# Kernel optimization log

Hardware: AMD Instinct MI355X
Metric: run time of the kernel (lower is better)

## Reference

```python
import jax, jax.numpy as jnp
import numpy as np

B, S, E, H = 4, 2048, 1024, 16
D = E // H  # head dim = 64


def setup_inputs() -> dict:
    key = jax.random.key(0)
    ks = jax.random.split(key, 9)
    sc = 1.0 / np.sqrt(E)
    x = jax.random.normal(ks[0], (B, S, E), dtype=jnp.float32)
    # causal mask: 1 = keep, 0 = masked -> -inf (matches masked_fill(mask==0, -inf))
    mask = jnp.broadcast_to(jnp.tril(jnp.ones((S, S), dtype=jnp.int32)), (B, S, S))
    return {
        "x": x,
        "mask": mask,
        "wq": jax.random.normal(ks[1], (E, E), dtype=jnp.float32) * sc,
        "bq": jax.random.normal(ks[2], (E,), dtype=jnp.float32) * sc,
        "wk": jax.random.normal(ks[3], (E, E), dtype=jnp.float32) * sc,
        "bk": jax.random.normal(ks[4], (E,), dtype=jnp.float32) * sc,
        "wv": jax.random.normal(ks[5], (E, E), dtype=jnp.float32) * sc,
        "bv": jax.random.normal(ks[6], (E,), dtype=jnp.float32) * sc,
        "wo": jax.random.normal(ks[7], (E, E), dtype=jnp.float32) * sc,
        "bo": jax.random.normal(ks[8], (E,), dtype=jnp.float32) * sc,
    }


def reference(x, mask, wq, bq, wk, bk, wv, bv, wo, bo):
    # nn.Linear: y = x @ W^T + b
    def proj(w, b):
        y = jnp.einsum('bse,fe->bsf', x, w) + b
        return y.reshape(B, S, H, D).transpose(0, 2, 1, 3)  # [B,H,S,D]

    q = proj(wq, bq)
    k = proj(wk, bk)
    v = proj(wv, bv)
    denom = jnp.asarray(np.sqrt(D), dtype=x.dtype)
    score = jnp.einsum('bhqd,bhkd->bhqk', q, k) / denom  # [B,H,S,S]
    score = jnp.where(mask[:, None, :, :] == 0, jnp.asarray(-jnp.inf, score.dtype), score)
    attn = jax.nn.softmax(score, axis=-1)
    out = jnp.einsum('bhqk,bhkd->bhqd', attn, v)  # [B,H,S,D]
    out = out.transpose(0, 2, 1, 3).reshape(B, S, E)
    return jnp.einsum('bse,fe->bsf', out, wo) + bo
```

## Files before the change

kernel.cpp:

```cpp
#include <hip/hip_runtime.h>
#include <cstdint>
#include <cstddef>

typedef unsigned short u16;
typedef __bf16 bf16;
typedef bf16 bf16x8 __attribute__((ext_vector_type(8)));
typedef bf16 bf16x4 __attribute__((ext_vector_type(4)));
typedef float f32x4 __attribute__((ext_vector_type(4)));
typedef u16 u16x8 __attribute__((ext_vector_type(8)));
typedef u16 u16x4 __attribute__((ext_vector_type(4)));

#define ASYNC16(g, l) __builtin_amdgcn_global_load_lds( \
    (const __attribute__((address_space(1))) void*)(g), \
    (__attribute__((address_space(3))) void*)(l), 16, 0, 0)

#define FENCE asm volatile("" ::: "memory")
#define BARRIER do { FENCE; __builtin_amdgcn_s_barrier(); FENCE; } while (0)
#define WAITVM(n) asm volatile("s_waitcnt vmcnt(" #n ")" ::: "memory")

__device__ __forceinline__ u16 f2bf(float f) {
  bf16 h = (bf16)f;
  return __builtin_bit_cast(u16, h);
}

__device__ __forceinline__ u16x4 pk4(float a, float b, float c, float d) {
  bf16x4 v = { (bf16)a, (bf16)b, (bf16)c, (bf16)d };
  return __builtin_bit_cast(u16x4, v);
}

__device__ __forceinline__ void store_out(u16* p, float v) { *p = f2bf(v); }
__device__ __forceinline__ void store_out(float* p, float v) { *p = v; }

__device__ __forceinline__ f32x4 mfma16(bf16x8 a, bf16x8 b, f32x4 c) {
  return __builtin_amdgcn_mfma_f32_16x16x32_bf16(a, b, c, 0, 0, 0);
}

__global__ void prep(const float* __restrict__ x,  const float* __restrict__ wq,
                     const float* __restrict__ wk, const float* __restrict__ wv,
                     const float* __restrict__ wo, const float* __restrict__ bq,
                     const float* __restrict__ bk,
                     u16* __restrict__ xb, u16* __restrict__ wqkb,
                     u16* __restrict__ wvb, u16* __restrict__ wob,
                     float* __restrict__ bqk, float scl)
{
  const int bid = blockIdx.x, tid = threadIdx.x;
  if (bid < 8192) {
    int i = bid * 256 + tid;
    float4 v = ((const float4*)x)[i];
    ((u16x4*)xb)[i] = pk4(v.x, v.y, v.z, v.w);
  } else if (bid < 12288) {
    int wsel = (bid - 8192) >> 10;
    int i = ((bid - 8192) & 1023) * 256 + tid;
    const float* src = wsel == 0 ? wq : wsel == 1 ? wk : wsel == 2 ? wv : wo;
    u16* dst = wsel == 0 ? wqkb : wsel == 1 ? wqkb + 1048576 : wsel == 2 ? wvb : wob;
    float s = wsel == 0 ? scl : 1.0f;
    float4 v = ((const float4*)src)[i];
    ((u16x4*)dst)[i] = pk4(v.x * s, v.y * s, v.z * s, v.w * s);
  } else {
    for (int i = tid; i < 1024; i += 256) {
      bqk[i] = bq[i] * scl;
      bqk[1024 + i] = bk[i];
    }
  }
}

template <typename OutT>
__device__ __forceinline__ void gemm128(
    u16* sA, u16* sB,
    const u16* __restrict__ A, const u16* __restrict__ Bm,
    const float* __restrict__ bias_col, const float* __restrict__ bias_row,
    OutT* __restrict__ C, int M, int N, int K, int bm, int bn)
{
  const int tid = threadIdx.x;
  const int w = tid >> 6, lane = tid & 63;
  const int quad = lane >> 4, l15 = lane & 15;
  const int wr = w >> 2, wc = w & 3;

  const int srow = tid >> 3;
  const int sslot = (tid & 7) ^ (srow & 7);
  const u16* gA = A + (size_t)(bm * 128 + srow) * K + sslot * 8;
  const u16* gB = Bm + (size_t)(bn * 256 + srow) * K + sslot * 8;
  u16* dA = sA + tid * 8;
  u16* dB = sB + tid * 8;
  const size_t rK64 = (size_t)64 * K;

  auto stage0 = [&](int c, int kt) {
    const u16* a = gA + kt * 64;
    u16* da = dA + c * 8192;
    ASYNC16(a, da);
    ASYNC16(a + rK64, da + 4096);
    ASYNC16(gB + kt * 64, dB + c * 16384);
  };
  auto stage1 = [&](int c, int kt) {
    const u16* b = gB + kt * 64;
    u16* db = dB + c * 16384;
    ASYNC16(b + rK64,     db + 4096);
    ASYNC16(b + 2 * rK64, db + 8192);
    ASYNC16(b + 3 * rK64, db + 12288);
  };

  f32x4 acc[4][4] = {};
  bf16x8 af[4][2];
  bf16x8 bfr[2][2];

  const int aRow = (wr * 64 + l15) * 64;
  const int bRow = (wc * 64 + l15) * 64;
  const int sw0 = (quad ^ (l15 & 7)) * 8;

#define LDA(SRC) do { \
    _Pragma("unroll") \
    for (int i = 0; i < 4; i++) { \
      af[i][0] = *(const bf16x8*)((SRC) + aRow + i * 1024 + sw0); \
      af[i][1] = *(const bf16x8*)((SRC) + aRow + i * 1024 + (sw0 ^ 32)); \
    } } while (0)

#define LDB(SRC, NH) do { \
    _Pragma("unroll") \
    for (int j = 0; j < 2; j++) { \
      bfr[j][0] = *(const bf16x8*)((SRC) + bRow + ((NH)*2 + j) * 1024 + sw0); \
      bfr[j][1] = *(const bf16x8*)((SRC) + bRow + ((NH)*2 + j) * 1024 + (sw0 ^ 32)); \
    } } while (0)

#define MMQ(NH) do { \
    __builtin_amdgcn_s_setprio(1); \
    _Pragma("unroll") \
    for (int i = 0; i < 4; i++) { \
      acc[i][(NH)*2+0] = mfma16(af[i][0], bfr[0][0], acc[i][(NH)*2+0]); \
      acc[i][(NH)*2+0] = mfma16(af[i][1], bfr[0][1], acc[i][(NH)*2+0]); \
      acc[i][(NH)*2+1] = mfma16(af[i][0], bfr[1][0], acc[i][(NH)*2+1]); \
      acc[i][(NH)*2+1] = mfma16(af[i][1], bfr[1][1], acc[i][(NH)*2+1]); \
    } \
    __builtin_amdgcn_s_setprio(0); \
  } while (0)

  const int NT = K >> 6;

  stage0(0, 0); stage1(0, 0);
  stage0(1, 1); stage1(1, 1);
  WAITVM(6);
  BARRIER;

  for (int t = 0; t < NT; ++t) {
    const int c = t % 3, c2 = (t + 2) % 3;
    const bool more = (t + 2 < NT);
    const u16* SA = sA + c * 8192;
    const u16* SB = sB + c * 16384;

    LDA(SA); LDB(SB, 0);
    if (more) stage0(c2, t + 2);
    BARRIER;
    MMQ(0);
    BARRIER;

    LDB(SB, 1);
    if (more) {
      stage1(c2, t + 2);
      WAITVM(6);
    } else if (t == NT - 2) {
      WAITVM(0);
    }
    BARRIER;
    MMQ(1);
    BARRIER;
  }

#pragma unroll
  for (int nh = 0; nh < 2; nh++) {
#pragma unroll
    for (int j = 0; j < 2; j++) {
      const int cc = bn * 256 + wc * 64 + nh * 32 + j * 16 + l15;
      const float bc = bias_col ? bias_col[cc] : 0.f;
#pragma unroll
      for (int i = 0; i < 4; i++) {
        const int r0 = bm * 128 + wr * 64 + i * 16 + quad * 4;
        f32x4 v = acc[i][nh * 2 + j];
#pragma unroll
        for (int ri = 0; ri < 4; ri++) {
          const float bb = bc + (bias_row ? bias_row[r0 + ri] : 0.f);
          store_out(&C[(size_t)(r0 + ri) * N + cc], v[ri] + bb);
        }
      }
    }
  }
#undef LDA
#undef LDB
#undef MMQ
}

__global__ __launch_bounds__(512, 2) void gemm_qkv(
    const u16* __restrict__ xb, const u16* __restrict__ wqkb,
    const u16* __restrict__ wvb, const float* __restrict__ bqk,
    const float* __restrict__ bv, u16* __restrict__ qk, u16* __restrict__ vt)
{
  __shared__ __align__(16) u16 sA[3 * 8192];
  __shared__ __align__(16) u16 sB[3 * 16384];
  const int id = blockIdx.x;
  if (id < 512) {
    gemm128<u16>(sA, sB, xb, wqkb, bqk, nullptr, qk, 8192, 2048, 1024,
                 id >> 3, id & 7);
  } else {
    const int j = id - 512;
    gemm128<u16>(sA, sB, wvb, xb, nullptr, bv, vt, 1024, 8192, 1024,
                 j & 7, j >> 3);
  }
}

__global__ __launch_bounds__(512, 2) void gemm_out(
    const u16* __restrict__ ctx, const u16* __restrict__ wob,
    const float* __restrict__ bo, float* __restrict__ out)
{
  __shared__ __align__(16) u16 sA[3 * 8192];
  __shared__ __align__(16) u16 sB[3 * 16384];
  const int id = blockIdx.x;
  gemm128<float>(sA, sB, ctx, wob, bo, nullptr, out, 8192, 1024, 1024,
                 id >> 2, id & 3);
}

__global__ __launch_bounds__(512, 2) void fattn(
    const u16* __restrict__ QK, const u16* __restrict__ VT, u16* __restrict__ ctx)
{
  __shared__ u16 Kt[2][128 * 64];
  __shared__ u16 Vt[2][64 * 128];
  __shared__ u16 Pt[8 * 32 * 32];

  const int tid = threadIdx.x;
  const int w = tid >> 6, lane = tid & 63;
  const int quad = lane >> 4, l15 = lane & 15;
  const int bx = blockIdx.x, h = blockIdx.y, b = blockIdx.z;
  const int P8[8] = {7, 0, 6, 1, 5, 2, 4, 3};
  const int tq = (b & 2) ? 7 - P8[bx] : P8[bx];
  const int qbase = tq * 256 + w * 32;

  const int kr = tid >> 3, kc = (tid & 7) ^ (kr & 7);
  const int vr = tid >> 4, vc = (tid & 15) ^ (vr & 15);

  const u16* QKb = QK + (size_t)b * 2048 * 2048;
  const u16* Kg = QKb + 1024 + h * 64 + kc * 8;
  const u16* Vg = VT + (size_t)(h * 64) * 8192 + b * 2048 + vc * 8;

  u16* Pw = Pt + w * 1024;

  bf16x8 ones;
#pragma unroll
  for (int j = 0; j < 8; j++) ones[j] = (bf16)1.0f;

  bf16x8 qf[2][2];
#pragma unroll
  for (int mt = 0; mt < 2; mt++)
#pragma unroll
    for (int ks = 0; ks < 2; ks++)
      qf[mt][ks] = *(const bf16x8*)(QKb + (size_t)(qbase + mt * 16 + l15) * 2048 +
                                    h * 64 + ks * 32 + quad * 8);

  auto stage = [&](int bi, int t) {
#pragma unroll
    for (int s = 0; s < 2; s++) {
      ASYNC16(Kg + (size_t)(t * 128 + s * 64 + kr) * 2048, Kt[bi] + (s * 512 + w * 64) * 8);
      ASYNC16(Vg + (size_t)(s * 32 + vr) * 8192 + t * 128,  Vt[bi] + (s * 512 + w * 64) * 8);
    }
  };

  f32x4 oacc[4][2] = {};
  f32x4 lacc[2] = {};

  const int tmax = 2 * tq + 1;
  stage(0, 0);

  for (int t = 0; t <= tmax; t++) {
    const int cur = t & 1;
    if (t < tmax) { stage(cur ^ 1, t + 1); WAITVM(4); }
    else          { WAITVM(0); }
    BARRIER;

    const u16* Kc = Kt[cur];
    const u16* Vc = Vt[cur];

    f32x4 st[2][8] = {};
#pragma unroll
    for (int ks = 0; ks < 2; ks++) {
      bf16x8 kf[8];
#pragma unroll
      for (int nt = 0; nt < 8; nt++) {
        int row = nt * 16 + l15;
        kf[nt] = *(const bf16x8*)(Kc + (row * 8 + ((ks * 4 + quad) ^ (row & 7))) * 8);
      }
#pragma unroll
      for (int nt = 0; nt < 8; nt++) {
        st[0][nt] = mfma16(kf[nt], qf[0][ks], st[0][nt]);
        st[1][nt] = mfma16(kf[nt], qf[1][ks], st[1][nt]);
      }
    }

    if (t >= 2 * tq) {
#pragma unroll
      for (int mt = 0; mt < 2; mt++) {
        const int qg = qbase + mt * 16 + l15;
#pragma unroll
        for (int nt = 0; nt < 8; nt++)
#pragma unroll
          for (int r = 0; r < 4; r++)
            if (t * 128 + nt * 16 + quad * 4 + r > qg) st[mt][nt][r] = -3e38f;
      }
    }
#pragma unroll
    for (int mt = 0; mt < 2; mt++)
#pragma unroll
      for (int nt = 0; nt < 8; nt++)
#pragma unroll
        for (int r = 0; r < 4; r++)
          st[mt][nt][r] = exp2f(st[mt][nt][r]);

#pragma unroll
    for (int hf = 0; hf < 2; hf++) {
#pragma unroll
      for (int ks = 0; ks < 2; ks++) {
#pragma unroll
        for (int mt = 0; mt < 2; mt++) {
          const int row = mt * 16 + l15;
          const int swz = (row >> 1) & 3;
#pragma unroll
          for (int j = 0; j < 2; j++) {
            int nt = hf * 4 + ks * 2 + j;
            u16x4 pkv = pk4(st[mt][nt][0], st[mt][nt][1], st[mt][nt][2], st[mt][nt][3]);
            int c = (j * 2 + (quad >> 1)) ^ swz;
            *(u16x4*)(Pw + (row << 5) + (c << 3) + ((quad & 1) << 2)) = pkv;
          }
        }
        const int cq = quad ^ ((l15 >> 1) & 3);
        bf16x8 pf0 = *(const bf16x8*)(Pw + (l15 << 5) + (cq << 3));
        bf16x8 pf1 = *(const bf16x8*)(Pw + ((16 + l15) << 5) + (cq << 3));
        lacc[0] = mfma16(ones, pf0, lacc[0]);
        lacc[1] = mfma16(ones, pf1, lacc[1]);
#pragma unroll
        for (int dt = 0; dt < 4; dt++) {
          int row = dt * 16 + l15;
          bf16x8 vf = *(const bf16x8*)(Vc + (row * 16 + ((hf * 8 + ks * 4 + quad) ^ (row & 15))) * 8);
          oacc[dt][0] = mfma16(vf, pf0, oacc[dt][0]);
          oacc[dt][1] = mfma16(vf, pf1, oacc[dt][1]);
        }
      }
    }
    BARRIER;
  }

#pragma unroll
  for (int mt = 0; mt < 2; mt++) {
    float rl = 1.0f / lacc[mt][0];
    size_t row = (size_t)b * 2048 + qbase + mt * 16 + l15;
#pragma unroll
    for (int dt = 0; dt < 4; dt++) {
      u16x4 o = pk4(oacc[dt][mt][0] * rl, oacc[dt][mt][1] * rl,
                    oacc[dt][mt][2] * rl, oacc[dt][mt][3] * rl);
      *(u16x4*)(ctx + row * 1024 + h * 64 + dt * 16 + quad * 4) = o;
    }
  }
}

extern "C" void kernel_launch(void* const* d_in, const int* in_sizes, int n_in,
                              void* d_out, int out_size, void* d_ws, size_t ws_size,
                              hipStream_t stream)
{
  const float* x  = (const float*)d_in[0];
  const float* wq = (const float*)d_in[2];
  const float* bq = (const float*)d_in[3];
  const float* wk = (const float*)d_in[4];
  const float* bk = (const float*)d_in[5];
  const float* wv = (const float*)d_in[6];
  const float* bv = (const float*)d_in[7];
  const float* wo = (const float*)d_in[8];
  const float* bo = (const float*)d_in[9];

  const float SCL = 0.125f * 1.44269504088896f;

  char* ws = (char*)d_ws;
  u16*   xb   = (u16*)(ws);
  u16*   ctx  = (u16*)(ws);
  u16*   wqkb = (u16*)(ws + 16777216);
  u16*   wvb  = (u16*)(ws + 20971520);
  u16*   wob  = (u16*)(ws + 23068672);
  float* bqk  = (float*)(ws + 25165824);
  u16*   qk   = (u16*)(ws + 25174016);
  u16*   vt   = (u16*)(ws + 58728448);
  float* out  = (float*)d_out;

  prep<<<12289, 256, 0, stream>>>(x, wq, wk, wv, wo, bq, bk,
                                  xb, wqkb, wvb, wob, bqk, SCL);

  gemm_qkv<<<768, 512, 0, stream>>>(xb, wqkb, wvb, bqk, bv, qk, vt);
  fattn<<<dim3(8, 16, 4), 512, 0, stream>>>(qk, vt, ctx);
  gemm_out<<<256, 512, 0, stream>>>(ctx, wob, bo, out);
}
```

Before: 313.9 us.

## Pair complementary 128-row query tiles per attention block for causal load balance

The flash-attention kernel now gives each block two 128-row query tiles, p and 15-p, processed back to back. Each block therefore runs a fixed 17 K/V iterations instead of a variable count that depended on its 256-row tile position. Each wave holds 16 query rows instead of 32, which halves register accumulators and the P scratch buffer. The aim is to remove the causal imbalance where the last-diagonal blocks set the critical path. In exchange, each K/V tile loaded into LDS is reused by half as many query rows.

```diff
diff --git a/kernel.cpp b/kernel.cpp
--- a/kernel.cpp
+++ b/kernel.cpp
@@ -221,15 +221,14 @@
 {
   __shared__ u16 Kt[2][128 * 64];
   __shared__ u16 Vt[2][64 * 128];
-  __shared__ u16 Pt[8 * 32 * 32];
+  __shared__ u16 Pt[8 * 16 * 32];
 
   const int tid = threadIdx.x;
   const int w = tid >> 6, lane = tid & 63;
   const int quad = lane >> 4, l15 = lane & 15;
-  const int bx = blockIdx.x, h = blockIdx.y, b = blockIdx.z;
-  const int P8[8] = {7, 0, 6, 1, 5, 2, 4, 3};
-  const int tq = (b & 2) ? 7 - P8[bx] : P8[bx];
-  const int qbase = tq * 256 + w * 32;
+  const int p = blockIdx.x, h = blockIdx.y, b = blockIdx.z;
+  const int nA = p + 1;
+  const int sBs = 15 - p;
 
   const int kr = tid >> 3, kc = (tid & 7) ^ (kr & 7);
   const int vr = tid >> 4, vc = (tid & 15) ^ (vr & 15);
@@ -238,19 +237,21 @@
   const u16* Kg = QKb + 1024 + h * 64 + kc * 8;
   const u16* Vg = VT + (size_t)(h * 64) * 8192 + b * 2048 + vc * 8;
 
-  u16* Pw = Pt + w * 1024;
+  u16* Pw = Pt + w * 512;
 
   bf16x8 ones;
 #pragma unroll
   for (int j = 0; j < 8; j++) ones[j] = (bf16)1.0f;
 
-  bf16x8 qf[2][2];
-#pragma unroll
-  for (int mt = 0; mt < 2; mt++)
-#pragma unroll
-    for (int ks = 0; ks < 2; ks++)
-      qf[mt][ks] = *(const bf16x8*)(QKb + (size_t)(qbase + mt * 16 + l15) * 2048 +
-                                    h * 64 + ks * 32 + quad * 8);
+  bf16x8 qfA[2], qfB[2], qcur[2];
+#pragma unroll
+  for (int ks = 0; ks < 2; ks++) {
+    qfA[ks] = *(const bf16x8*)(QKb + (size_t)(p  * 128 + w * 16 + l15) * 2048 +
+                               h * 64 + ks * 32 + quad * 8);
+    qfB[ks] = *(const bf16x8*)(QKb + (size_t)(sBs * 128 + w * 16 + l15) * 2048 +
+                               h * 64 + ks * 32 + quad * 8);
+  }
+  qcur[0] = qfA[0]; qcur[1] = qfA[1];
 
   auto stage = [&](int bi, int t) {
 #pragma unroll
@@ -260,22 +261,38 @@
     }
   };
 
-  f32x4 oacc[4][2] = {};
-  f32x4 lacc[2] = {};
-
-  const int tmax = 2 * tq + 1;
+  f32x4 oacc[4] = {};
+  f32x4 lacc = {};
+
+  auto epi = [&](int sIdx) {
+    float rl = 1.0f / lacc[0];
+    size_t row = (size_t)b * 2048 + sIdx * 128 + w * 16 + l15;
+#pragma unroll
+    for (int dt = 0; dt < 4; dt++) {
+      u16x4 o = pk4(oacc[dt][0] * rl, oacc[dt][1] * rl,
+                    oacc[dt][2] * rl, oacc[dt][3] * rl);
+      *(u16x4*)(ctx + row * 1024 + h * 64 + dt * 16 + quad * 4) = o;
+    }
+  };
+
+  int sCur = p, tcur = 0;
   stage(0, 0);
 
-  for (int t = 0; t <= tmax; t++) {
-    const int cur = t & 1;
-    if (t < tmax) { stage(cur ^ 1, t + 1); WAITVM(4); }
-    else          { WAITVM(0); }
+  for (int u = 0; u < 17; ++u) {
+    const int cur = u & 1;
+    if (u < 16) {
+      const int tn = (u + 1 == nA) ? 0 : tcur + 1;
+      stage(cur ^ 1, tn);
+      WAITVM(4);
+    } else {
+      WAITVM(0);
+    }
     BARRIER;
 
     const u16* Kc = Kt[cur];
     const u16* Vc = Vt[cur];
 
-    f32x4 st[2][8] = {};
+    f32x4 st[8] = {};
 #pragma unroll
     for (int ks = 0; ks < 2; ks++) {
       bf16x8 kf[8];
@@ -285,75 +302,62 @@
         kf[nt] = *(const bf16x8*)(Kc + (row * 8 + ((ks * 4 + quad) ^ (row & 7))) * 8);
       }
 #pragma unroll
-      for (int nt = 0; nt < 8; nt++) {
-        st[0][nt] = mfma16(kf[nt], qf[0][ks], st[0][nt]);
-        st[1][nt] = mfma16(kf[nt], qf[1][ks], st[1][nt]);
-      }
-    }
-
-    if (t >= 2 * tq) {
-#pragma unroll
-      for (int mt = 0; mt < 2; mt++) {
-        const int qg = qbase + mt * 16 + l15;
-#pragma unroll
-        for (int nt = 0; nt < 8; nt++)
-#pragma unroll
-          for (int r = 0; r < 4; r++)
-            if (t * 128 + nt * 16 + quad * 4 + r > qg) st[mt][nt][r] = -3e38f;
-      }
-    }
-#pragma unroll
-    for (int mt = 0; mt < 2; mt++)
-#pragma unroll
       for (int nt = 0; nt < 8; nt++)
+        st[nt] = mfma16(kf[nt], qcur[ks], st[nt]);
+    }
+
+    if (tcur == sCur) {
+      const int qg = w * 16 + l15;
+#pragma unroll
+      for (int nt = 0; nt < 8; nt++)
 #pragma unroll
         for (int r = 0; r < 4; r++)
-          st[mt][nt][r] = exp2f(st[mt][nt][r]);
-
+          if (nt * 16 + quad * 4 + r > qg) st[nt][r] = -3e38f;
+    }
+#pragma unroll
+    for (int nt = 0; nt < 8; nt++)
+#pragma unroll
+      for (int r = 0; r < 4; r++)
+        st[nt][r] = exp2f(st[nt][r]);
+
+    const int swz = (l15 >> 1) & 3;
 #pragma unroll
     for (int hf = 0; hf < 2; hf++) {
 #pragma unroll
       for (int ks = 0; ks < 2; ks++) {
 #pragma unroll
-        for (int mt = 0; mt < 2; mt++) {
-          const int row = mt * 16 + l15;
-          const int swz = (row >> 1) & 3;
-#pragma unroll
-          for (int j = 0; j < 2; j++) {
-            int nt = hf * 4 + ks * 2 + j;
-            u16x4 pkv = pk4(st[mt][nt][0], st[mt][nt][1], st[mt][nt][2], st[mt][nt][3]);
-            int c = (j * 2 + (quad >> 1)) ^ swz;
-            *(u16x4*)(Pw + (row << 5) + (c << 3) + ((quad & 1) << 2)) = pkv;
-          }
+        for (int j = 0; j < 2; j++) {
+          int nt = hf * 4 + ks * 2 + j;
+          u16x4 pkv = pk4(st[nt][0], st[nt][1], st[nt][2], st[nt][3]);
+          int c = (j * 2 + (quad >> 1)) ^ swz;
+          *(u16x4*)(Pw + (l15 << 5) + (c << 3) + ((quad & 1) << 2)) = pkv;
         }
-        const int cq = quad ^ ((l15 >> 1) & 3);
+        const int cq = quad ^ swz;
         bf16x8 pf0 = *(const bf16x8*)(Pw + (l15 << 5) + (cq << 3));
-        bf16x8 pf1 = *(const bf16x8*)(Pw + ((16 + l15) << 5) + (cq << 3));
-        lacc[0] = mfma16(ones, pf0, lacc[0]);
-        lacc[1] = mfma16(ones, pf1, lacc[1]);
+        lacc = mfma16(ones, pf0, lacc);
 #pragma unroll
         for (int dt = 0; dt < 4; dt++) {
-          int row = dt * 16 + l15;
-          bf16x8 vf = *(const bf16x8*)(Vc + (row * 16 + ((hf * 8 + ks * 4 + quad) ^ (row & 15))) * 8);
-          oacc[dt][0] = mfma16(vf, pf0, oacc[dt][0]);
-          oacc[dt][1] = mfma16(vf, pf1, oacc[dt][1]);
+          int vrow = dt * 16 + l15;
+          bf16x8 vf = *(const bf16x8*)(Vc + (vrow * 16 + ((hf * 8 + ks * 4 + quad) ^ (vrow & 15))) * 8);
+          oacc[dt] = mfma16(vf, pf0, oacc[dt]);
         }
       }
     }
     BARRIER;
-  }
-
-#pragma unroll
-  for (int mt = 0; mt < 2; mt++) {
-    float rl = 1.0f / lacc[mt][0];
-    size_t row = (size_t)b * 2048 + qbase + mt * 16 + l15;
-#pragma unroll
-    for (int dt = 0; dt < 4; dt++) {
-      u16x4 o = pk4(oacc[dt][mt][0] * rl, oacc[dt][mt][1] * rl,
-                    oacc[dt][mt][2] * rl, oacc[dt][mt][3] * rl);
-      *(u16x4*)(ctx + row * 1024 + h * 64 + dt * 16 + quad * 4) = o;
-    }
-  }
+
+    if (u == nA - 1) {
+      epi(p);
+#pragma unroll
+      for (int dt = 0; dt < 4; dt++) oacc[dt] = f32x4{0.f, 0.f, 0.f, 0.f};
+      lacc = f32x4{0.f, 0.f, 0.f, 0.f};
+      qcur[0] = qfB[0]; qcur[1] = qfB[1];
+      sCur = sBs; tcur = 0;
+    } else {
+      tcur++;
+    }
+  }
+
+  epi(sBs);
 }
 
 extern "C" void kernel_launch(void* const* d_in, const int* in_sizes, int n_in,
```

Result: faster. 304.7 us (-2.9%).
